# Performance work log

Hardware: AMD Instinct MI355X
Metric: run time of the kernel (lower is better)

## Reference

```python
import jax, jax.numpy as jnp
import numpy as np

B, S, E, H, C = 64, 512, 768, 768, 9
Q_GCE = 0.7
TAU = 0.7
IGNORE = -100


def setup_inputs() -> dict:
    key = jax.random.key(0)
    k_h, k_w1, k_w2, k_lab, k_drop = jax.random.split(key, 5)
    hidden = jax.random.normal(k_h, (B, S, E), dtype=jnp.float32)
    W1 = jax.random.normal(k_w1, (E, H), dtype=jnp.float32) * (1.0 / np.sqrt(E))
    b1 = jnp.zeros((H,), dtype=jnp.float32)
    W2 = jax.random.normal(k_w2, (H, C), dtype=jnp.float32) * (1.0 / np.sqrt(H))
    b2 = jnp.zeros((C,), dtype=jnp.float32)
    labels = jax.random.randint(k_lab, (B, S), 0, C, dtype=jnp.int64 if jax.config.jax_enable_x64 else jnp.int32)
    drop = jax.random.uniform(k_drop, (B, S)) < 0.1
    labels = jnp.where(drop, IGNORE, labels)
    return {"hidden": hidden, "W1": W1, "b1": b1, "W2": W2, "b2": b2,
            "labels": labels, "epoch": 5}


def reference(hidden, W1, b1, W2, b2, labels, epoch):
    # head: Linear -> Tanh -> Linear (dropout is identity at eval)
    h = jnp.tanh(jnp.einsum('bse,eh->bsh', hidden, W1) + b1)
    logit = jnp.einsum('bsh,hc->bsc', h, W2) + b2
    probs = jax.nn.softmax(logit, axis=2)  # [B,S,C]

    mask = labels != IGNORE
    safe_labels = jnp.where(mask, labels, 0)
    # p_i = probs[i, labels[i]] gathered for every token
    p = jnp.take_along_axis(probs, safe_labels[..., None], axis=2)[..., 0]  # [B,S]
    # GCE weight: w=1 for epoch<=2, else 1 if p>tau else 0 (constant wrt grads)
    w = jnp.where(epoch <= 2, 1.0, jnp.where(p > TAU, 1.0, 0.0))
    w = jax.lax.stop_gradient(w) * mask.astype(probs.dtype)
    loss = jnp.sum(w * (1.0 - jnp.power(p, Q_GCE)) / Q_GCE)
    return probs, loss
```

## Files before the change

kernel.cpp:

```cpp
#include <hip/hip_runtime.h>
#include <hip/hip_bf16.h>
#include <stdint.h>

#define E_ 768
#define H_ 768
#define C_ 9
#define M_TOTAL 32768
#define BM_ 64

typedef __attribute__((ext_vector_type(8))) __bf16 bf16x8;
typedef __attribute__((ext_vector_type(4))) float f32x4;
typedef __attribute__((ext_vector_type(4))) int i32x4;

static_assert(sizeof(bf16x8) == 16, "bf16x8 must be 16B");

__device__ __forceinline__ unsigned short f2bf(float f) {
    __hip_bfloat16 h = __float2bfloat16(f);
    return __builtin_bit_cast(unsigned short, h);
}

__global__ void prep_kernel(const float* __restrict__ W1, const float* __restrict__ W2,
                            unsigned short* __restrict__ W1f, unsigned short* __restrict__ W2f,
                            float* __restrict__ loss_out)
{
    int b = blockIdx.x;
    int n = threadIdx.x;
    if (b < 768) {
        int k = b;
        float v = W1[k * H_ + n];
        int ntile = n >> 4;
        int t = k >> 5;
        int lane = (n & 15) + 16 * ((k >> 3) & 3);
        int j = k & 7;
        W1f[((ntile * 24 + t) * 64 + lane) * 8 + j] = f2bf(v);
    } else {
        for (int it = 0; it < 16; ++it) {
            int tid = it * 768 + n;
            int j    = tid & 7;
            int lane = (tid >> 3) & 63;
            int t    = tid >> 9;
            int cls  = lane & 15;
            int k = t * 32 + (lane >> 4) * 8 + j;
            W2f[tid] = (cls < C_) ? f2bf(W2[k * C_ + cls]) : (unsigned short)0;
        }
        if (n == 0) *loss_out = 0.0f;
    }
}

__launch_bounds__(1024, 4)
__global__ void fused_head_kernel(const float* __restrict__ hidden,
                                  const unsigned short* __restrict__ W1f,
                                  const float* __restrict__ b1,
                                  const unsigned short* __restrict__ W2f,
                                  const float* __restrict__ b2,
                                  const int* __restrict__ labels,
                                  const int* __restrict__ epoch_p,
                                  float* __restrict__ probs,
                                  float* __restrict__ loss)
{
    __shared__ unsigned short Ash[24 * 4 * 512];

    const int tid  = threadIdx.x;
    const int w    = tid >> 6;
    const int lane = tid & 63;
    const int tok0 = blockIdx.x * BM_;
    const int c16  = lane & 15;
    const int q    = lane >> 4;

    const f32x4* hsrc = (const f32x4*)(hidden + (size_t)tok0 * E_);
    const int tkA = tid >> 5;
    const int fq  = tid & 31;
    const int t_l = fq >> 3;
    const int jj  = (fq & 1) * 4;
    const int q2s = (fq >> 1) & 3;

    f32x4 rg0, rg1;
    auto issue = [&](int c) {
        rg0 = __builtin_nontemporal_load(hsrc + (size_t)tkA * 192 + c * 32 + fq);
        rg1 = __builtin_nontemporal_load(hsrc + (size_t)(tkA + 32) * 192 + c * 32 + fq);
    };
    auto stage = [&](int bsel) {
        unsigned short* bufp = &Ash[bsel * 8192];
        {
            int lnf = (tkA & 15) + 16 * q2s;
            int mt  = tkA >> 4;
            ushort4 pk = { f2bf(rg0[0]), f2bf(rg0[1]), f2bf(rg0[2]), f2bf(rg0[3]) };
            *(ushort4*)(&bufp[((t_l * 4 + mt) * 64 + lnf) * 8 + jj]) = pk;
        }
        {
            int tk  = tkA + 32;
            int lnf = (tk & 15) + 16 * q2s;
            int mt  = tk >> 4;
            ushort4 pk = { f2bf(rg1[0]), f2bf(rg1[1]), f2bf(rg1[2]), f2bf(rg1[3]) };
            *(ushort4*)(&bufp[((t_l * 4 + mt) * 64 + lnf) * 8 + jj]) = pk;
        }
    };

    issue(0);

    const unsigned short* Wp = W1f + (size_t)(w * 3 * 24) * 512 + lane * 8;
    bf16x8 b0[3], b1v_[3];
    #pragma unroll
    for (int i = 0; i < 3; ++i)
        b0[i] = __builtin_bit_cast(bf16x8, *(const i32x4*)(Wp + (i * 24 + 0) * 512));
    #pragma unroll
    for (int i = 0; i < 3; ++i)
        b1v_[i] = __builtin_bit_cast(bf16x8, *(const i32x4*)(Wp + (i * 24 + 1) * 512));

    const f32x4 zero4 = {0.0f, 0.0f, 0.0f, 0.0f};
    f32x4 acc[4][3];
    #pragma unroll
    for (int mt = 0; mt < 4; ++mt)
        #pragma unroll
        for (int nt = 0; nt < 3; ++nt) acc[mt][nt] = zero4;

    stage(0);
    asm volatile("s_waitcnt lgkmcnt(0)\ns_barrier" ::: "memory");

    bf16x8 af[2][4];
    {
        const unsigned short* bufp = &Ash[0];
        #pragma unroll
        for (int mt = 0; mt < 4; ++mt)
            af[0][mt] = __builtin_bit_cast(bf16x8,
                *(const i32x4*)(&bufp[((0 * 4 + mt) * 64 + lane) * 8]));
    }

    #pragma unroll
    for (int c = 0; c < 6; ++c) {
        const unsigned short* bufp = &Ash[(c & 1) * 8192];
        if (c < 5) issue(c + 1);
        #pragma unroll
        for (int tl = 0; tl < 4; ++tl) {
            const int tt = 4 * c + tl;
            const int cur = tl & 1;
            if (tl < 3) {
                #pragma unroll
                for (int mt = 0; mt < 4; ++mt)
                    af[cur ^ 1][mt] = __builtin_bit_cast(bf16x8,
                        *(const i32x4*)(&bufp[(((tl + 1) * 4 + mt) * 64 + lane) * 8]));
            }
            __builtin_amdgcn_s_setprio(1);
            if ((tt & 1) == 0) {
                #pragma unroll
                for (int mt = 0; mt < 4; ++mt)
                    #pragma unroll
                    for (int nt = 0; nt < 3; ++nt)
                        acc[mt][nt] = __builtin_amdgcn_mfma_f32_16x16x32_bf16(
                            af[cur][mt], b0[nt], acc[mt][nt], 0, 0, 0);
            } else {
                #pragma unroll
                for (int mt = 0; mt < 4; ++mt)
                    #pragma unroll
                    for (int nt = 0; nt < 3; ++nt)
                        acc[mt][nt] = __builtin_amdgcn_mfma_f32_16x16x32_bf16(
                            af[cur][mt], b1v_[nt], acc[mt][nt], 0, 0, 0);
            }
            __builtin_amdgcn_s_setprio(0);
            if (tt + 2 < 24) {
                if ((tt & 1) == 0) {
                    #pragma unroll
                    for (int i = 0; i < 3; ++i)
                        b0[i] = __builtin_bit_cast(bf16x8,
                            *(const i32x4*)(Wp + (i * 24 + tt + 2) * 512));
                } else {
                    #pragma unroll
                    for (int i = 0; i < 3; ++i)
                        b1v_[i] = __builtin_bit_cast(bf16x8,
                            *(const i32x4*)(Wp + (i * 24 + tt + 2) * 512));
                }
            }
            if (tl == 1 && c < 5) stage((c + 1) & 1);
        }
        asm volatile("s_waitcnt lgkmcnt(0)\ns_barrier" ::: "memory");
        if (c < 5) {
            const unsigned short* bufn = &Ash[((c + 1) & 1) * 8192];
            #pragma unroll
            for (int mt = 0; mt < 4; ++mt)
                af[0][mt] = __builtin_bit_cast(bf16x8,
                    *(const i32x4*)(&bufn[((0 * 4 + mt) * 64 + lane) * 8]));
        }
    }

    unsigned short* Hsh = &Ash[0];
    #pragma unroll
    for (int i = 0; i < 3; ++i) {
        int col = w * 48 + i * 16 + c16;
        float b1b = b1[col];
        int t2 = col >> 5;
        int q2 = (col >> 3) & 3;
        int j  = col & 7;
        #pragma unroll
        for (int mt = 0; mt < 4; ++mt) {
            #pragma unroll
            for (int r = 0; r < 4; ++r) {
                float z = acc[mt][i][r] + b1b;
                float e = exp2f(z * 2.8853900817779268f);
                float th = 1.0f - 2.0f * __builtin_amdgcn_rcpf(e + 1.0f);
                int lanep = (q * 4 + r) + 16 * q2;
                Hsh[((t2 * 4 + mt) * 64 + lanep) * 8 + j] = f2bf(th);
            }
        }
    }
    asm volatile("s_waitcnt lgkmcnt(0)\ns_barrier" ::: "memory");

    if (w < 4) {
        f32x4 logit = zero4;
        #pragma unroll
        for (int t2 = 0; t2 < 24; ++t2) {
            bf16x8 ha = __builtin_bit_cast(bf16x8, *(const i32x4*)(&Hsh[((t2 * 4 + w) * 64 + lane) * 8]));
            bf16x8 wb = __builtin_bit_cast(bf16x8, *(const i32x4*)(W2f + ((size_t)t2 * 64 + lane) * 8));
            logit = __builtin_amdgcn_mfma_f32_16x16x32_bf16(ha, wb, logit, 0, 0, 0);
        }

        const bool valid = (c16 < C_);
        const float b2v = valid ? b2[c16] : 0.0f;
        const int ep = epoch_p[0];
        float lsum = 0.0f;
        #pragma unroll
        for (int r = 0; r < 4; ++r) {
            float l = valid ? (logit[r] + b2v) : -3.0e38f;
            float m = l;
            #pragma unroll
            for (int d = 1; d < 16; d <<= 1)
                m = fmaxf(m, __shfl_xor(m, d, 64));
            float e = valid ? exp2f((l - m) * 1.44269504f) : 0.0f;
            float s = e;
            #pragma unroll
            for (int d = 1; d < 16; d <<= 1)
                s += __shfl_xor(s, d, 64);
            float p = e / s;
            int row = tok0 + w * 16 + q * 4 + r;
            if (valid) __builtin_nontemporal_store(p, &probs[(size_t)row * C_ + c16]);
            int lab = labels[row];
            if (valid && lab == c16) {
                float wgt = (ep <= 2) ? 1.0f : ((p > 0.7f) ? 1.0f : 0.0f);
                if (wgt > 0.0f)
                    lsum += (1.0f - exp2f(0.7f * log2f(p))) * (1.0f / 0.7f);
            }
        }
        #pragma unroll
        for (int d = 1; d < 64; d <<= 1)
            lsum += __shfl_xor(lsum, d, 64);
        if (lane == 0) atomicAdd(loss, lsum);
    }
}

extern "C" void kernel_launch(void* const* d_in, const int* in_sizes, int n_in,
                              void* d_out, int out_size, void* d_ws, size_t ws_size,
                              hipStream_t stream)
{
    const float* hidden = (const float*)d_in[0];
    const float* W1     = (const float*)d_in[1];
    const float* b1     = (const float*)d_in[2];
    const float* W2     = (const float*)d_in[3];
    const float* b2     = (const float*)d_in[4];
    const int*   labels = (const int*)d_in[5];
    const int*   epoch  = (const int*)d_in[6];

    float* probs = (float*)d_out;
    float* loss  = probs + (size_t)M_TOTAL * C_;

    unsigned short* W1f = (unsigned short*)d_ws;
    unsigned short* W2f = W1f + 48 * 24 * 512;

    prep_kernel<<<769, 768, 0, stream>>>(W1, W2, W1f, W2f, loss);
    fused_head_kernel<<<M_TOTAL / BM_, 1024, 0, stream>>>(hidden, W1f, b1, W2f, b2,
                                                          labels, epoch, probs, loss);
}
```

Before: 214.6 us.

## Stagger per-wave K-order in GEMM and vectorize W1 prep stores

The main kernel now has each wave walk the four K sub-tiles of every staged chunk in a rotated order based on its wave index. The goal is to spread LDS reads of the A fragments and global reads of W1 across different addresses, reducing bank and channel contention. The prep kernel is also rewritten so each thread gathers eight W1 values and writes one 16-byte packed store, with the block count and block size changed to match. The rotated order makes the indexing of the double-buffered B fragments more intricate, and the accumulation order now differs per wave.

Result: slower. 252.6 us (+17.7%).

```diff
diff --git a/kernel.cpp b/kernel.cpp
--- a/kernel.cpp
+++ b/kernel.cpp
@@ -25,17 +25,26 @@
 {
     int b = blockIdx.x;
     int n = threadIdx.x;
-    if (b < 768) {
-        int k = b;
-        float v = W1[k * H_ + n];
-        int ntile = n >> 4;
-        int t = k >> 5;
-        int lane = (n & 15) + 16 * ((k >> 3) & 3);
-        int j = k & 7;
-        W1f[((ntile * 24 + t) * 64 + lane) * 8 + j] = f2bf(v);
+    if (b < 288) {
+        int cell = b * 256 + n;
+        int lane = cell & 63;
+        int t    = (cell >> 6) % 24;
+        int nt   = cell / 1536;
+        int col  = nt * 16 + (lane & 15);
+        int q2   = (lane >> 4) & 3;
+        const float* src = W1 + (size_t)(t * 32 + q2 * 8) * H_ + col;
+        int d[4];
+        #pragma unroll
+        for (int jj = 0; jj < 4; ++jj) {
+            unsigned int lo = f2bf(src[(2 * jj)     * H_]);
+            unsigned int hi = f2bf(src[(2 * jj + 1) * H_]);
+            d[jj] = (int)(lo | (hi << 16));
+        }
+        i32x4 v = { d[0], d[1], d[2], d[3] };
+        *(i32x4*)(W1f + (size_t)cell * 8) = v;
     } else {
-        for (int it = 0; it < 16; ++it) {
-            int tid = it * 768 + n;
+        for (int it = 0; it < 48; ++it) {
+            int tid = it * 256 + n;
             int j    = tid & 7;
             int lane = (tid >> 3) & 63;
             int t    = tid >> 9;
@@ -63,6 +72,7 @@
     const int tid  = threadIdx.x;
     const int w    = tid >> 6;
     const int lane = tid & 63;
+    const int w4   = w & 3;
     const int tok0 = blockIdx.x * BM_;
     const int c16  = lane & 15;
     const int q    = lane >> 4;
@@ -88,7 +98,7 @@
             *(ushort4*)(&bufp[((t_l * 4 + mt) * 64 + lnf) * 8 + jj]) = pk;
         }
         {
-            int tk  = tkA + 32;
+            int tk = tkA + 32;
             int lnf = (tk & 15) + 16 * q2s;
             int mt  = tk >> 4;
             ushort4 pk = { f2bf(rg1[0]), f2bf(rg1[1]), f2bf(rg1[2]), f2bf(rg1[3]) };
@@ -99,13 +109,17 @@
     issue(0);
 
     const unsigned short* Wp = W1f + (size_t)(w * 3 * 24) * 512 + lane * 8;
-    bf16x8 b0[3], b1v_[3];
-    #pragma unroll
-    for (int i = 0; i < 3; ++i)
-        b0[i] = __builtin_bit_cast(bf16x8, *(const i32x4*)(Wp + (i * 24 + 0) * 512));
-    #pragma unroll
-    for (int i = 0; i < 3; ++i)
-        b1v_[i] = __builtin_bit_cast(bf16x8, *(const i32x4*)(Wp + (i * 24 + 1) * 512));
+    bf16x8 bA[3], bB[3];
+    {
+        int g0 = w4;
+        int g1 = (1 + w4) & 3;
+        #pragma unroll
+        for (int i = 0; i < 3; ++i)
+            bA[i] = __builtin_bit_cast(bf16x8, *(const i32x4*)(Wp + (i * 24 + g0) * 512));
+        #pragma unroll
+        for (int i = 0; i < 3; ++i)
+            bB[i] = __builtin_bit_cast(bf16x8, *(const i32x4*)(Wp + (i * 24 + g1) * 512));
+    }
 
     const f32x4 zero4 = {0.0f, 0.0f, 0.0f, 0.0f};
     f32x4 acc[4][3];
@@ -123,7 +137,7 @@
         #pragma unroll
         for (int mt = 0; mt < 4; ++mt)
             af[0][mt] = __builtin_bit_cast(bf16x8,
-                *(const i32x4*)(&bufp[((0 * 4 + mt) * 64 + lane) * 8]));
+                *(const i32x4*)(&bufp[((w4 * 4 + mt) * 64 + lane) * 8]));
     }
 
     #pragma unroll
@@ -131,46 +145,48 @@
         const unsigned short* bufp = &Ash[(c & 1) * 8192];
         if (c < 5) issue(c + 1);
         #pragma unroll
-        for (int tl = 0; tl < 4; ++tl) {
-            const int tt = 4 * c + tl;
-            const int cur = tl & 1;
-            if (tl < 3) {
+        for (int p = 0; p < 4; ++p) {
+            const int cur = p & 1;
+            if (p < 3) {
+                int kkn = (p + 1 + w4) & 3;
                 #pragma unroll
                 for (int mt = 0; mt < 4; ++mt)
                     af[cur ^ 1][mt] = __builtin_bit_cast(bf16x8,
-                        *(const i32x4*)(&bufp[(((tl + 1) * 4 + mt) * 64 + lane) * 8]));
+                        *(const i32x4*)(&bufp[((kkn * 4 + mt) * 64 + lane) * 8]));
             }
             __builtin_amdgcn_s_setprio(1);
-            if ((tt & 1) == 0) {
+            if (cur == 0) {
                 #pragma unroll
                 for (int mt = 0; mt < 4; ++mt)
                     #pragma unroll
                     for (int nt = 0; nt < 3; ++nt)
                         acc[mt][nt] = __builtin_amdgcn_mfma_f32_16x16x32_bf16(
-                            af[cur][mt], b0[nt], acc[mt][nt], 0, 0, 0);
+                            af[cur][mt], bA[nt], acc[mt][nt], 0, 0, 0);
             } else {
                 #pragma unroll
                 for (int mt = 0; mt < 4; ++mt)
                     #pragma unroll
                     for (int nt = 0; nt < 3; ++nt)
                         acc[mt][nt] = __builtin_amdgcn_mfma_f32_16x16x32_bf16(
-                            af[cur][mt], b1v_[nt], acc[mt][nt], 0, 0, 0);
+                            af[cur][mt], bB[nt], acc[mt][nt], 0, 0, 0);
             }
             __builtin_amdgcn_s_setprio(0);
-            if (tt + 2 < 24) {
-                if ((tt & 1) == 0) {
+            if (4 * c + p + 2 < 24) {
+                const int gc = c + ((p + 2) >> 2);
+                int g = 4 * gc + ((((p + 2) & 3) + w4) & 3);
+                if (cur == 0) {
                     #pragma unroll
                     for (int i = 0; i < 3; ++i)
-                        b0[i] = __builtin_bit_cast(bf16x8,
-                            *(const i32x4*)(Wp + (i * 24 + tt + 2) * 512));
+                        bA[i] = __builtin_bit_cast(bf16x8,
+                            *(const i32x4*)(Wp + (i * 24 + g) * 512));
                 } else {
                     #pragma unroll
                     for (int i = 0; i < 3; ++i)
-                        b1v_[i] = __builtin_bit_cast(bf16x8,
-                            *(const i32x4*)(Wp + (i * 24 + tt + 2) * 512));
+                        bB[i] = __builtin_bit_cast(bf16x8,
+                            *(const i32x4*)(Wp + (i * 24 + g) * 512));
                 }
             }
-            if (tl == 1 && c < 5) stage((c + 1) & 1);
+            if (p == 1 && c < 5) stage((c + 1) & 1);
         }
         asm volatile("s_waitcnt lgkmcnt(0)\ns_barrier" ::: "memory");
         if (c < 5) {
@@ -178,7 +194,7 @@
             #pragma unroll
             for (int mt = 0; mt < 4; ++mt)
                 af[0][mt] = __builtin_bit_cast(bf16x8,
-                    *(const i32x4*)(&bufn[((0 * 4 + mt) * 64 + lane) * 8]));
+                    *(const i32x4*)(&bufn[((w4 * 4 + mt) * 64 + lane) * 8]));
         }
     }
 
@@ -264,7 +280,7 @@
     unsigned short* W1f = (unsigned short*)d_ws;
     unsigned short* W2f = W1f + 48 * 24 * 512;
 
-    prep_kernel<<<769, 768, 0, stream>>>(W1, W2, W1f, W2f, loss);
+    prep_kernel<<<289, 256, 0, stream>>>(W1, W2, W1f, W2f, loss);
     fused_head_kernel<<<M_TOTAL / BM_, 1024, 0, stream>>>(hidden, W1f, b1, W2f, b2,
                                                           labels, epoch, probs, loss);
 }
```
